# Optimization experiments

Hardware: AMD Instinct MI355X
Metric: run time of the kernel (lower is better)

Reference implementation:

```python
import jax, jax.numpy as jnp
import numpy as np

DIM = 512
H = 8
HD = DIM // H
MAXREL = 8
BF16_MIN = -3.3895313892515355e38  # torch.finfo(torch.bfloat16).min


def setup_inputs() -> dict:
    key = jax.random.key(0)
    k1, k2, k3, k4, k5, k6 = jax.random.split(key, 6)
    b, l, n, d = 4, 16, 64, DIM
    x = jax.random.normal(k1, (b, l, n, d), dtype=jnp.float32)
    time_embeddings = jax.random.normal(k2, (b, l, d), dtype=jnp.float32)
    # relative frame positions in [-MAXREL, MAXREL]
    pos = jax.random.randint(k3, (b, l, l), 0, 2 * MAXREL + 1) - MAXREL
    pos = pos.astype(jnp.int64) if jax.config.read('jax_enable_x64') else pos.astype(jnp.int32)
    # causal mask over frames
    mask = jnp.tril(jnp.ones((l, l), dtype=jnp.int32))[None].repeat(b, axis=0)
    # params (torch Linear convention: out = x @ W.T)
    W_qkv = jax.random.normal(k4, (3 * d, d), dtype=jnp.float32) * (1.0 / np.sqrt(d))
    W_tqkv = jax.random.normal(k5, (3 * HD, d), dtype=jnp.float32) * (1.0 / np.sqrt(d))
    # xavier_uniform for embeddings table [2*max+1, head_dim]
    lim = np.sqrt(6.0 / (2 * MAXREL + 1 + HD))
    emb_table = jax.random.uniform(k6, (2 * MAXREL + 1, HD), minval=-lim, maxval=lim, dtype=jnp.float32)
    return {"x": x, "time_embeddings": time_embeddings, "pos": pos, "mask": mask,
            "W_qkv": W_qkv, "W_tqkv": W_tqkv, "emb_table": emb_table}


def _forward(x, time_embeddings, pos, mask, W_qkv, W_tqkv, emb_table):
    b, l, n, d = x.shape
    h, hd = H, HD
    N = l * n
    scale = np.sqrt(d).astype(np.float32)

    qkv = jnp.einsum('blnd,ed->blne', x, W_qkv)
    q, k, v = jnp.split(qkv, 3, axis=-1)

    def to_heads(t):  # [b,l,n,d] -> [b,h,l,n,hd]
        return t.reshape(b, l, n, h, hd).transpose(0, 3, 1, 2, 4)
    q, k, v = to_heads(q), to_heads(k), to_heads(v)

    # time qkv: [b,l,3*hd] -> broadcast add over heads and tokens
    tqkv = jnp.einsum('bld,ed->ble', time_embeddings, W_tqkv)
    qt, kt, vt = jnp.split(tqkv, 3, axis=-1)  # each [b,l,hd]

    def add_t(t, tt):  # tt: [b,l,hd] -> [b,1,l,1,hd]
        return t + tt[:, None, :, None, :]
    q = add_t(q, qt).reshape(b, h, N, hd)
    k = add_t(k, kt).reshape(b, h, N, hd)
    v = add_t(v, vt).reshape(b, h, N, hd)

    # content scores [b,h,N,N]
    qk = jnp.einsum('bhqd,bhkd->bhqk', q, k)

    # relative position bias
    idx = jnp.clip(pos, -MAXREL, MAXREL) + MAXREL          # [b,l,l]
    emb = emb_table[idx]                                    # [b,l,l,hd]
    # q chunked: [b,h,(l n),hd] -> [b,h,n,l,hd] (l is major in (l n))
    qc = q.reshape(b, h, l, n, hd).transpose(0, 1, 3, 2, 4)
    qr = jnp.einsum('bhnqd,bqkd->bhqnk', qc, emb)           # [b,h,l,n,l]
    qr = jnp.broadcast_to(qr[..., None], (b, h, l, n, l, n)).reshape(b, h, N, N)

    attn = (qk + qr) / scale

    # expand frame mask [b,l,l] -> [b,N,N]
    exp_mask = jnp.broadcast_to(mask[:, :, None, :, None], (b, l, n, l, n)).reshape(b, N, N)
    attn = jnp.where(exp_mask[:, None] == 0, BF16_MIN, attn)

    attn = jax.nn.softmax(attn, axis=-1)
    out = jnp.einsum('bhqk,bhkd->bhqd', attn, v)            # [b,h,N,hd]
    out = out.reshape(b, h, l, n, hd).transpose(0, 2, 3, 1, 4).reshape(b, l, n, d)
    return out


def reference(x, time_embeddings, pos, mask, W_qkv, W_tqkv, emb_table):
    return _forward(x, time_embeddings, pos, mask, W_qkv, W_tqkv, emb_table)
```

## Files before the change

### kernel.cpp

```cpp
#include <hip/hip_runtime.h>

typedef unsigned short u16;
typedef __attribute__((ext_vector_type(8))) short short8;
typedef __attribute__((ext_vector_type(4))) float f32x4;
typedef __attribute__((ext_vector_type(4))) u16 u16x4;

#define BB 4
#define LL 16
#define DD 512
#define NH 8
#define HDIM 64
#define NSEQ 1024
#define E3 1536
#define INV_SCALE 0.04419417382415922f

__device__ __forceinline__ u16 f2bf(float f) {
  union { float f; unsigned u; } v; v.f = f;
  unsigned u = v.u;
  unsigned r = u + 0x7fffu + ((u >> 16) & 1u);
  return (u16)(r >> 16);
}

__device__ __forceinline__ unsigned cvtpk(float lo, float hi) {
  unsigned r;
  asm("v_cvt_pk_bf16_f32 %0, %1, %2" : "=v"(r) : "v"(lo), "v"(hi));
  return r;
}

__device__ __forceinline__ uint4 pack8(float4 a, float4 b) {
  uint4 r;
  r.x = (unsigned)f2bf(a.x) | ((unsigned)f2bf(a.y) << 16);
  r.y = (unsigned)f2bf(a.z) | ((unsigned)f2bf(a.w) << 16);
  r.z = (unsigned)f2bf(b.x) | ((unsigned)f2bf(b.y) << 16);
  r.w = (unsigned)f2bf(b.z) | ((unsigned)f2bf(b.w) << 16);
  return r;
}

__device__ __forceinline__ void stage16(const u16* g, u16* l) {
  __builtin_amdgcn_global_load_lds((const __attribute__((address_space(1))) unsigned int*)g,
                                   (__attribute__((address_space(3))) unsigned int*)l,
                                   16, 0, 0);
}

__global__ __launch_bounds__(256) void prep_tproj(const float* __restrict__ x,
                                                  const float* __restrict__ w,
                                                  const float* __restrict__ te,
                                                  const float* __restrict__ wt,
                                                  u16* __restrict__ xbf,
                                                  u16* __restrict__ wbf,
                                                  float* __restrict__ tq) {
  __shared__ u16 At[64][72];
  __shared__ u16 Bt[64][72];
  const int nx = (4096 * DD) / 4;
  const int nw = (E3 * DD) / 4;
  int blk = blockIdx.x;
  int tid = threadIdx.x;

  if (blk < 2816) {
    int i = blk * 256 + tid;
    const float4* src;
    uint2* dst;
    int j;
    if (i < nx) { src = (const float4*)x; dst = (uint2*)xbf; j = i; }
    else { src = (const float4*)w; dst = (uint2*)wbf; j = i - nx; }
    float4 v = src[j];
    unsigned lo = (unsigned)f2bf(v.x) | ((unsigned)f2bf(v.y) << 16);
    unsigned hi = (unsigned)f2bf(v.z) | ((unsigned)f2bf(v.w) << 16);
    dst[j] = make_uint2(lo, hi);
    return;
  }

  int bn = blk - 2816;
  int w_ = tid >> 6, l = tid & 63;
  int l15 = l & 15, l16 = l >> 4;
  int r0 = tid >> 3, c0 = (tid & 7) * 8;
  f32x4 acc[4] = {};
  for (int kt = 0; kt < DD; kt += 64) {
    {
      const float* ta = &te[(size_t)r0 * DD + kt + c0];
      const float* tb = &te[(size_t)(r0 + 32) * DD + kt + c0];
      *(uint4*)&At[r0][c0]      = pack8(*(const float4*)ta, *(const float4*)(ta + 4));
      *(uint4*)&At[r0 + 32][c0] = pack8(*(const float4*)tb, *(const float4*)(tb + 4));
      const float* wa = &wt[(size_t)(bn * 64 + r0) * DD + kt + c0];
      const float* wb_ = &wt[(size_t)(bn * 64 + r0 + 32) * DD + kt + c0];
      *(uint4*)&Bt[r0][c0]      = pack8(*(const float4*)wa, *(const float4*)(wa + 4));
      *(uint4*)&Bt[r0 + 32][c0] = pack8(*(const float4*)wb_, *(const float4*)(wb_ + 4));
    }
    __syncthreads();
#pragma unroll
    for (int ks = 0; ks < 2; ++ks) {
      short8 bfr = *(const short8*)&Bt[w_ * 16 + l15][ks * 32 + l16 * 8];
#pragma unroll
      for (int mt = 0; mt < 4; ++mt) {
        short8 afr = *(const short8*)&At[mt * 16 + l15][ks * 32 + l16 * 8];
        acc[mt] = __builtin_amdgcn_mfma_f32_16x16x32_bf16(afr, bfr, acc[mt], 0, 0, 0);
      }
    }
    __syncthreads();
  }
  int e = bn * 64 + w_ * 16 + l15;
#pragma unroll
  for (int mt = 0; mt < 4; ++mt)
#pragma unroll
    for (int r = 0; r < 4; ++r)
      tq[(mt * 16 + l16 * 4 + r) * 192 + e] = acc[mt][r];
}

__global__ __launch_bounds__(256) void gemm_qkv(const u16* __restrict__ xb,
                                                const u16* __restrict__ wb,
                                                const float* __restrict__ tq,
                                                u16* __restrict__ qp,
                                                u16* __restrict__ kp,
                                                u16* __restrict__ vt) {
  __shared__ u16 As[2][128][72];
  __shared__ u16 Bs[2][128][72];
  int bn = blockIdx.x;
  int bm = blockIdx.y;
  int tid = threadIdx.x;
  int w = tid >> 6, l = tid & 63;
  int wr = w >> 1, wc = w & 1;
  int l15 = l & 15, l16 = l >> 4;
  int r0 = tid >> 3, c0 = (tid & 7) * 8;

  f32x4 acc[4][4] = {};
  uint4 ra[4], rb[4];

#define LOADT(kt)                                                                    \
  {                                                                                  \
    _Pragma("unroll") for (int c = 0; c < 4; ++c) {                                  \
      ra[c] = *(const uint4*)&xb[(size_t)(bm * 128 + c * 32 + r0) * DD + (kt) + c0]; \
      rb[c] = *(const uint4*)&wb[(size_t)(bn * 128 + c * 32 + r0) * DD + (kt) + c0]; \
    }                                                                                \
  }
#define STORET(buf)                                                                  \
  {                                                                                  \
    _Pragma("unroll") for (int c = 0; c < 4; ++c) {                                  \
      *(uint4*)&As[buf][c * 32 + r0][c0] = ra[c];                                    \
      *(uint4*)&Bs[buf][c * 32 + r0][c0] = rb[c];                                    \
    }                                                                                \
  }

  LOADT(0);
  STORET(0);
  __syncthreads();
  int cur = 0;
#pragma unroll
  for (int i = 0; i < 8; ++i) {
    if (i < 7) LOADT((i + 1) * 64);
#pragma unroll
    for (int ks = 0; ks < 2; ++ks) {
      short8 af[4], bf[4];
#pragma unroll
      for (int mt = 0; mt < 4; ++mt)
        af[mt] = *(const short8*)&As[cur][wr * 64 + mt * 16 + l15][ks * 32 + l16 * 8];
#pragma unroll
      for (int nt = 0; nt < 4; ++nt)
        bf[nt] = *(const short8*)&Bs[cur][wc * 64 + nt * 16 + l15][ks * 32 + l16 * 8];
#pragma unroll
      for (int mt = 0; mt < 4; ++mt)
#pragma unroll
        for (int nt = 0; nt < 4; ++nt)
          acc[mt][nt] = __builtin_amdgcn_mfma_f32_16x16x32_bf16(af[mt], bf[nt], acc[mt][nt], 0, 0, 0);
    }
    if (i < 7) STORET(cur ^ 1);
    __syncthreads();
    cur ^= 1;
  }
#undef LOADT
#undef STORET

  int part = bn >> 2;
  int frame = bm * 2 + wr;
  const float* tqrow = &tq[frame * 192 + part * 64];
  float tvals[4];
#pragma unroll
  for (int nt = 0; nt < 4; ++nt) tvals[nt] = tqrow[nt * 16 + l15];

  u16 (*E)[136] = (u16(*)[136])(&As[0][0][0]);

  if (part == 2) {
#pragma unroll
    for (int mt = 0; mt < 4; ++mt)
#pragma unroll
      for (int nt = 0; nt < 4; ++nt)
#pragma unroll
        for (int r = 0; r < 4; ++r)
          E[wc * 64 + nt * 16 + l15][wr * 64 + mt * 16 + l16 * 4 + r] = f2bf(acc[mt][nt][r] + tvals[nt]);
  } else {
#pragma unroll
    for (int mt = 0; mt < 4; ++mt)
#pragma unroll
      for (int nt = 0; nt < 4; ++nt)
#pragma unroll
        for (int r = 0; r < 4; ++r)
          E[wr * 64 + mt * 16 + l16 * 4 + r][wc * 64 + nt * 16 + l15] = f2bf(acc[mt][nt][r] + tvals[nt]);
  }
  __syncthreads();

  int rlane = tid & 15;
  int b0 = bm >> 3;
  if (part == 2) {
#pragma unroll
    for (int pass = 0; pass < 8; ++pass) {
      int e = pass * 16 + (tid >> 4);
      int din = (bn & 3) * 128 + e;
      int hh = din >> 6, hd = din & 63;
      uint4 vv = *(const uint4*)&E[e][rlane * 8];
      size_t base = ((size_t)(b0 * NH + hh) * HDIM + hd) * NSEQ + (bm & 7) * 128 + rlane * 8;
      *(uint4*)&vt[base] = vv;
    }
  } else {
    u16* dst = (part == 0) ? qp : kp;
#pragma unroll
    for (int pass = 0; pass < 8; ++pass) {
      int m = pass * 16 + (tid >> 4);
      int e = rlane * 8;
      int din = (bn & 3) * 128 + e;
      int hh = din >> 6, hd = din & 63;
      int nn0 = (bm & 7) * 128 + m;
      uint4 vv = *(const uint4*)&E[m][e];
      *(uint4*)&dst[((size_t)(b0 * NH + hh) * NSEQ + nn0) * HDIM + hd] = vv;
    }
  }
}

__global__ __launch_bounds__(128, 2) void attn_kernel(const u16* __restrict__ qp,
                                                      const u16* __restrict__ kp,
                                                      const u16* __restrict__ vt,
                                                      const int* __restrict__ pos,
                                                      const float* __restrict__ emb,
                                                      float* __restrict__ out) {
  __shared__ __align__(16) u16 Kt[2][64][64];
  __shared__ __align__(16) u16 Vt[2][64][64];

  int blk = blockIdx.x;
  int qf = 15 - (blk >> 6);
  int bhid = (blk >> 1) & 31;
  int half = blk & 1;
  int b = bhid >> 3, h = bhid & 7;
  int tid = threadIdx.x;
  int rg = tid >> 6;
  int l = tid & 63;
  int l15 = l & 15, l16 = l >> 4;
  int srow = l >> 3, c8 = l & 7;
  int schunk = c8 ^ srow;
  int swzA = (l15 & 7) << 4;
  int rga = half * 2 + rg;

  size_t bh = (size_t)(b * NH + h);
  const u16* Kb = kp + bh * NSEQ * HDIM;
  const u16* Vb = vt + bh * HDIM * NSEQ;
  int rowl0 = rg * 16 + srow;
  int rowl1 = rowl0 + 8;

#define STAGE(kf_, buf_)                                                       \
  {                                                                            \
    stage16(Kb + ((kf_) * 64 + rowl0) * HDIM + schunk * 8,                     \
            &Kt[buf_][rg * 16 + 0][0] + l * 8);                                \
    stage16(Kb + ((kf_) * 64 + rowl1) * HDIM + schunk * 8,                     \
            &Kt[buf_][rg * 16 + 8][0] + l * 8);                                \
    stage16(Kb + ((kf_) * 64 + rowl0 + 32) * HDIM + schunk * 8,                \
            &Kt[buf_][rg * 16 + 32][0] + l * 8);                               \
    stage16(Kb + ((kf_) * 64 + rowl1 + 32) * HDIM + schunk * 8,                \
            &Kt[buf_][rg * 16 + 40][0] + l * 8);                               \
    stage16(Vb + (size_t)rowl0 * NSEQ + (kf_) * 64 + schunk * 8,               \
            &Vt[buf_][rg * 16 + 0][0] + l * 8);                                \
    stage16(Vb + (size_t)rowl1 * NSEQ + (kf_) * 64 + schunk * 8,               \
            &Vt[buf_][rg * 16 + 8][0] + l * 8);                                \
    stage16(Vb + (size_t)(rowl0 + 32) * NSEQ + (kf_) * 64 + schunk * 8,        \
            &Vt[buf_][rg * 16 + 32][0] + l * 8);                               \
    stage16(Vb + (size_t)(rowl1 + 32) * NSEQ + (kf_) * 64 + schunk * 8,        \
            &Vt[buf_][rg * 16 + 40][0] + l * 8);                               \
  }

  const u16* Qg = qp + (bh * NSEQ + qf * 64 + rga * 16) * HDIM;
  short8 aq[2];
  aq[0] = *(const short8*)&Qg[l15 * HDIM + l16 * 8];
  aq[1] = *(const short8*)&Qg[l15 * HDIM + 32 + l16 * 8];

  STAGE(0, 0);
  if (qf > 0) STAGE(1, 1);

  int pp = pos[(b * LL + qf) * LL + l15];
  pp = (pp < -8 ? -8 : (pp > 8 ? 8 : pp)) + 8;
  const float* ev = emb + pp * HDIM;
  f32x4 bfragT = {};
#pragma unroll
  for (int ks = 0; ks < 2; ++ks) {
    float4 e0 = *(const float4*)&ev[ks * 32 + l16 * 8];
    float4 e1 = *(const float4*)&ev[ks * 32 + l16 * 8 + 4];
    short8 ef;
    ef[0] = (short)f2bf(e0.x); ef[1] = (short)f2bf(e0.y);
    ef[2] = (short)f2bf(e0.z); ef[3] = (short)f2bf(e0.w);
    ef[4] = (short)f2bf(e1.x); ef[5] = (short)f2bf(e1.y);
    ef[6] = (short)f2bf(e1.z); ef[7] = (short)f2bf(e1.w);
    bfragT = __builtin_amdgcn_mfma_f32_16x16x32_bf16(ef, aq[ks], bfragT, 0, 0, 0);
  }

  f32x4 o[4] = {};
  float lsum = 0.f;

  if (qf > 0) { asm volatile("s_waitcnt vmcnt(8)" ::: "memory"); }
  else        { asm volatile("s_waitcnt vmcnt(0)" ::: "memory"); }
  __syncthreads();

  for (int kf = 0; kf <= qf; ++kf) {
    int cur = kf & 1;
    const char* ktb = (const char*)&Kt[cur][0][0];
    const char* vtb = (const char*)&Vt[cur][0][0];

    f32x4 s[4] = {};
    __builtin_amdgcn_s_setprio(1);
#pragma unroll
    for (int ks = 0; ks < 2; ++ks)
#pragma unroll
      for (int nt = 0; nt < 4; ++nt) {
        short8 kfrag = *(const short8*)(ktb + (nt * 16 + l15) * 128 + ((ks * 64 + l16 * 16) ^ swzA));
        s[nt] = __builtin_amdgcn_mfma_f32_16x16x32_bf16(kfrag, aq[ks], s[nt], 0, 0, 0);
      }
    __builtin_amdgcn_s_setprio(0);

    float bb = __shfl(bfragT[kf & 3], ((kf >> 2) << 4) | l15) * INV_SCALE;

    float pv[4][4];
#pragma unroll
    for (int nt = 0; nt < 4; ++nt)
#pragma unroll
      for (int r = 0; r < 4; ++r) {
        float p = __expf(fmaf(s[nt][r], INV_SCALE, bb));
        pv[nt][r] = p;
        lsum += p;
      }

#pragma unroll
    for (int w32 = 0; w32 < 2; ++w32) {
      union { unsigned u[4]; short8 s8; } pf;
      pf.u[0] = cvtpk(pv[w32 * 2][0], pv[w32 * 2][1]);
      pf.u[1] = cvtpk(pv[w32 * 2][2], pv[w32 * 2][3]);
      pf.u[2] = cvtpk(pv[w32 * 2 + 1][0], pv[w32 * 2 + 1][1]);
      pf.u[3] = cvtpk(pv[w32 * 2 + 1][2], pv[w32 * 2 + 1][3]);
      int off0 = w32 * 64 + l16 * 8;
      int cp = off0 & ~15, sub = off0 & 15;
      __builtin_amdgcn_s_setprio(1);
#pragma unroll
      for (int dt = 0; dt < 4; ++dt) {
        int d = dt * 16 + l15;
        int sx = (d & 7) << 4;
        union { uint2 h2[2]; short8 s8; } vf;
        vf.h2[0] = *(const uint2*)(vtb + d * 128 + (cp ^ sx) + sub);
        vf.h2[1] = *(const uint2*)(vtb + d * 128 + ((cp + 32) ^ sx) + sub);
        o[dt] = __builtin_amdgcn_mfma_f32_16x16x32_bf16(vf.s8, pf.s8, o[dt], 0, 0, 0);
      }
      __builtin_amdgcn_s_setprio(0);
    }

    if (kf < qf) {
      __syncthreads();
      if (kf + 2 <= qf) {
        STAGE(kf + 2, cur);
        asm volatile("s_waitcnt vmcnt(8)" ::: "memory");
      } else {
        asm volatile("s_waitcnt vmcnt(0)" ::: "memory");
      }
      __syncthreads();
    }
  }
#undef STAGE

  lsum += __shfl_xor(lsum, 16);
  lsum += __shfl_xor(lsum, 32);
  float inv = 1.0f / lsum;

  float* outp = out + ((size_t)(b * LL + qf) * 64 + rga * 16) * DD + h * 64;
#pragma unroll
  for (int dt = 0; dt < 4; ++dt) {
    float4 v;
    v.x = o[dt][0] * inv; v.y = o[dt][1] * inv;
    v.z = o[dt][2] * inv; v.w = o[dt][3] * inv;
    *(float4*)&outp[(size_t)l15 * DD + dt * 16 + l16 * 4] = v;
  }
}

extern "C" void kernel_launch(void* const* d_in, const int* in_sizes, int n_in,
                              void* d_out, int out_size, void* d_ws, size_t ws_size,
                              hipStream_t stream) {
  const float* x    = (const float*)d_in[0];
  const float* te   = (const float*)d_in[1];
  const int*   pos  = (const int*)d_in[2];
  const float* wqkv = (const float*)d_in[4];
  const float* wt   = (const float*)d_in[5];
  const float* emb  = (const float*)d_in[6];
  float* out = (float*)d_out;
  char* ws = (char*)d_ws;

  const size_t OFF_XBF = 0;
  const size_t OFF_WBF  = OFF_XBF + (size_t)4096 * DD * 2;
  const size_t OFF_TQ   = OFF_WBF + (size_t)E3 * DD * 2;
  const size_t OFF_QKV  = OFF_TQ + (size_t)64 * 192 * 4;
  const size_t PLANE = (size_t)BB * NH * NSEQ * HDIM;

  u16*   xbf  = (u16*)(ws + OFF_XBF);
  u16*   wbf  = (u16*)(ws + OFF_WBF);
  float* tq   = (float*)(ws + OFF_TQ);
  u16*   qpl  = (u16*)(ws + OFF_QKV);
  u16*   kpl  = qpl + PLANE;
  u16*   vtl  = qpl + 2 * PLANE;

  prep_tproj<<<2819, 256, 0, stream>>>(x, wqkv, te, wt, xbf, wbf, tq);
  gemm_qkv<<<dim3(12, 32), 256, 0, stream>>>(xbf, wbf, tq, qpl, kpl, vtl);
  attn_kernel<<<1024, 128, 0, stream>>>(qpl, kpl, vtl, pos, emb, out);
}
```

Baseline: 116.8 us.

## Fuse fp32-to-bf16 conversion into QKV GEMM tile loads, drop prep pass

Removes the separate pass that converted x and W_qkv to bf16 in workspace. The QKV GEMM now loads fp32 tiles directly and packs them to bf16 with v_cvt_pk_bf16_f32 before storing to LDS, and the time projection becomes its own small 3-block kernel. This saves a full write and re-read of the bf16 copies. In exchange each GEMM tile load moves twice the bytes, weights are re-converted by every block that reads them, and register pressure rises from holding float4 pairs.

Result: slower. 123.1 us (+5.4%).

```diff
diff --git a/kernel.cpp b/kernel.cpp
--- a/kernel.cpp
+++ b/kernel.cpp
@@ -29,10 +29,10 @@
 
 __device__ __forceinline__ uint4 pack8(float4 a, float4 b) {
   uint4 r;
-  r.x = (unsigned)f2bf(a.x) | ((unsigned)f2bf(a.y) << 16);
-  r.y = (unsigned)f2bf(a.z) | ((unsigned)f2bf(a.w) << 16);
-  r.z = (unsigned)f2bf(b.x) | ((unsigned)f2bf(b.y) << 16);
-  r.w = (unsigned)f2bf(b.z) | ((unsigned)f2bf(b.w) << 16);
+  r.x = cvtpk(a.x, a.y);
+  r.y = cvtpk(a.z, a.w);
+  r.z = cvtpk(b.x, b.y);
+  r.w = cvtpk(b.z, b.w);
   return r;
 }
 
@@ -42,36 +42,14 @@
                                    16, 0, 0);
 }
 
-__global__ __launch_bounds__(256) void prep_tproj(const float* __restrict__ x,
-                                                  const float* __restrict__ w,
-                                                  const float* __restrict__ te,
+__global__ __launch_bounds__(256) void tproj_mfma(const float* __restrict__ te,
                                                   const float* __restrict__ wt,
-                                                  u16* __restrict__ xbf,
-                                                  u16* __restrict__ wbf,
                                                   float* __restrict__ tq) {
   __shared__ u16 At[64][72];
   __shared__ u16 Bt[64][72];
-  const int nx = (4096 * DD) / 4;
-  const int nw = (E3 * DD) / 4;
-  int blk = blockIdx.x;
+  int bn = blockIdx.x;
   int tid = threadIdx.x;
-
-  if (blk < 2816) {
-    int i = blk * 256 + tid;
-    const float4* src;
-    uint2* dst;
-    int j;
-    if (i < nx) { src = (const float4*)x; dst = (uint2*)xbf; j = i; }
-    else { src = (const float4*)w; dst = (uint2*)wbf; j = i - nx; }
-    float4 v = src[j];
-    unsigned lo = (unsigned)f2bf(v.x) | ((unsigned)f2bf(v.y) << 16);
-    unsigned hi = (unsigned)f2bf(v.z) | ((unsigned)f2bf(v.w) << 16);
-    dst[j] = make_uint2(lo, hi);
-    return;
-  }
-
-  int bn = blk - 2816;
-  int w_ = tid >> 6, l = tid & 63;
+  int w = tid >> 6, l = tid & 63;
   int l15 = l & 15, l16 = l >> 4;
   int r0 = tid >> 3, c0 = (tid & 7) * 8;
   f32x4 acc[4] = {};
@@ -89,7 +67,7 @@
     __syncthreads();
 #pragma unroll
     for (int ks = 0; ks < 2; ++ks) {
-      short8 bfr = *(const short8*)&Bt[w_ * 16 + l15][ks * 32 + l16 * 8];
+      short8 bfr = *(const short8*)&Bt[w * 16 + l15][ks * 32 + l16 * 8];
 #pragma unroll
       for (int mt = 0; mt < 4; ++mt) {
         short8 afr = *(const short8*)&At[mt * 16 + l15][ks * 32 + l16 * 8];
@@ -98,7 +76,7 @@
     }
     __syncthreads();
   }
-  int e = bn * 64 + w_ * 16 + l15;
+  int e = bn * 64 + w * 16 + l15;
 #pragma unroll
   for (int mt = 0; mt < 4; ++mt)
 #pragma unroll
@@ -106,8 +84,8 @@
       tq[(mt * 16 + l16 * 4 + r) * 192 + e] = acc[mt][r];
 }
 
-__global__ __launch_bounds__(256) void gemm_qkv(const u16* __restrict__ xb,
-                                                const u16* __restrict__ wb,
+__global__ __launch_bounds__(256) void gemm_qkv(const float* __restrict__ xf,
+                                                const float* __restrict__ wf,
                                                 const float* __restrict__ tq,
                                                 u16* __restrict__ qp,
                                                 u16* __restrict__ kp,
@@ -123,21 +101,25 @@
   int r0 = tid >> 3, c0 = (tid & 7) * 8;
 
   f32x4 acc[4][4] = {};
-  uint4 ra[4], rb[4];
-
-#define LOADT(kt)                                                                    \
-  {                                                                                  \
-    _Pragma("unroll") for (int c = 0; c < 4; ++c) {                                  \
-      ra[c] = *(const uint4*)&xb[(size_t)(bm * 128 + c * 32 + r0) * DD + (kt) + c0]; \
-      rb[c] = *(const uint4*)&wb[(size_t)(bn * 128 + c * 32 + r0) * DD + (kt) + c0]; \
-    }                                                                                \
-  }
-#define STORET(buf)                                                                  \
-  {                                                                                  \
-    _Pragma("unroll") for (int c = 0; c < 4; ++c) {                                  \
-      *(uint4*)&As[buf][c * 32 + r0][c0] = ra[c];                                    \
-      *(uint4*)&Bs[buf][c * 32 + r0][c0] = rb[c];                                    \
-    }                                                                                \
+  float4 ra[4][2], rb[4][2];
+
+#define LOADT(kt)                                                                      \
+  {                                                                                    \
+    _Pragma("unroll") for (int c = 0; c < 4; ++c) {                                    \
+      const float* pa = &xf[(size_t)(bm * 128 + c * 32 + r0) * DD + (kt) + c0];        \
+      ra[c][0] = *(const float4*)pa;                                                   \
+      ra[c][1] = *(const float4*)(pa + 4);                                             \
+      const float* pb = &wf[(size_t)(bn * 128 + c * 32 + r0) * DD + (kt) + c0];        \
+      rb[c][0] = *(const float4*)pb;                                                   \
+      rb[c][1] = *(const float4*)(pb + 4);                                             \
+    }                                                                                  \
+  }
+#define STORET(buf)                                                                    \
+  {                                                                                    \
+    _Pragma("unroll") for (int c = 0; c < 4; ++c) {                                    \
+      *(uint4*)&As[buf][c * 32 + r0][c0] = pack8(ra[c][0], ra[c][1]);                  \
+      *(uint4*)&Bs[buf][c * 32 + r0][c0] = pack8(rb[c][0], rb[c][1]);                  \
+    }                                                                                  \
   }
 
   LOADT(0);
@@ -393,20 +375,16 @@
   float* out = (float*)d_out;
   char* ws = (char*)d_ws;
 
-  const size_t OFF_XBF = 0;
-  const size_t OFF_WBF  = OFF_XBF + (size_t)4096 * DD * 2;
-  const size_t OFF_TQ   = OFF_WBF + (size_t)E3 * DD * 2;
-  const size_t OFF_QKV  = OFF_TQ + (size_t)64 * 192 * 4;
+  const size_t OFF_TQ  = 0;
+  const size_t OFF_QKV = OFF_TQ + (size_t)64 * 192 * 4;
   const size_t PLANE = (size_t)BB * NH * NSEQ * HDIM;
 
-  u16*   xbf  = (u16*)(ws + OFF_XBF);
-  u16*   wbf  = (u16*)(ws + OFF_WBF);
   float* tq   = (float*)(ws + OFF_TQ);
   u16*   qpl  = (u16*)(ws + OFF_QKV);
   u16*   kpl  = qpl + PLANE;
   u16*   vtl  = qpl + 2 * PLANE;
 
-  prep_tproj<<<2819, 256, 0, stream>>>(x, wqkv, te, wt, xbf, wbf, tq);
-  gemm_qkv<<<dim3(12, 32), 256, 0, stream>>>(xbf, wbf, tq, qpl, kpl, vtl);
+  tproj_mfma<<<3, 256, 0, stream>>>(te, wt, tq);
+  gemm_qkv<<<dim3(12, 32), 256, 0, stream>>>(x, wqkv, tq, qpl, kpl, vtl);
   attn_kernel<<<1024, 128, 0, stream>>>(qpl, kpl, vtl, pos, emb, out);
 }
```
